# Performance work log

Measured on AMD Instinct MI355X. Metric: run time of the kernel, lower is better.

## Reference

```python
import jax, jax.numpy as jnp
import numpy as np

C = 512; H = 64; W = 64; STRIDE = 16; NA = 9; IMG = 1024
PRE_NMS = 6000; POST_NMS = 300; NMS_T = 0.7; MIN_SIZE = 16.0
BBOX_CLIP = float(np.log(1000.0 / 16.0))  # standard dw/dh clamp for exp() safety


def _make_anchors():
    # 3 scales x 3 aspect ratios on a stride-16 grid -> (H*W*9, 4) xyxy anchors
    scales = np.array([128.0, 256.0, 512.0])
    ratios = np.array([0.5, 1.0, 2.0])
    hs = (scales[:, None] * np.sqrt(ratios)[None, :]).ravel()
    ws = (scales[:, None] / np.sqrt(ratios)[None, :]).ravel()
    yy, xx = np.meshgrid((np.arange(H) + 0.5) * STRIDE, (np.arange(W) + 0.5) * STRIDE, indexing='ij')
    ctr = np.stack([xx.ravel(), yy.ravel()], -1)            # (HW, 2) centers
    wh = np.stack([ws, hs], -1)                              # (9, 2)
    anc = np.concatenate([ctr[:, None, :] - 0.5 * wh[None], ctr[:, None, :] + 0.5 * wh[None]], -1)
    return anc.reshape(-1, 4).astype(np.float32)             # (HW*9, 4)


def setup_inputs() -> dict:
    key = jax.random.key(0)
    k = jax.random.split(key, 4)
    return {
        'feature_map': jax.random.normal(k[0], (1, C, H, W), jnp.float32),
        'anchors': jnp.asarray(_make_anchors()),
        'image_shape': jnp.array([IMG, IMG], jnp.int32),
        'conv1_w': 0.01 * jax.random.normal(k[1], (C, C, 3, 3), jnp.float32),
        'conv1_b': jnp.zeros((C,), jnp.float32),
        'cls_w': 0.01 * jax.random.normal(k[2], (NA, C, 1, 1), jnp.float32),
        'cls_b': jnp.zeros((NA,), jnp.float32),
        'box_w': 0.01 * jax.random.normal(k[3], (NA * 4, C, 1, 1), jnp.float32),
        'box_b': jnp.zeros((NA * 4,), jnp.float32),
    }


def _conv(x, w, b):
    dn = ('NCHW', 'OIHW', 'NCHW')
    return jax.lax.conv_general_dilated(x, w, (1, 1), 'SAME', dimension_numbers=dn) + b[None, :, None, None]


def _decode_boxes(deltas, anchors):
    aw = anchors[:, 2] - anchors[:, 0]
    ah = anchors[:, 3] - anchors[:, 1]
    ax = anchors[:, 0] + 0.5 * aw
    ay = anchors[:, 1] + 0.5 * ah
    dx, dy, dw, dh = deltas[:, 0], deltas[:, 1], deltas[:, 2], deltas[:, 3]
    dw = jnp.minimum(dw, BBOX_CLIP)
    dh = jnp.minimum(dh, BBOX_CLIP)
    px = dx * aw + ax
    py = dy * ah + ay
    pw = jnp.exp(dw) * aw
    ph = jnp.exp(dh) * ah
    return jnp.stack([px - 0.5 * pw, py - 0.5 * ph, px + 0.5 * pw, py + 0.5 * ph], -1)


def _pairwise_iou(a, b):
    area_a = (a[:, 2] - a[:, 0]) * (a[:, 3] - a[:, 1])
    area_b = (b[:, 2] - b[:, 0]) * (b[:, 3] - b[:, 1])
    lt = jnp.maximum(a[:, None, :2], b[None, :, :2])
    rb = jnp.minimum(a[:, None, 2:], b[None, :, 2:])
    wh = jnp.clip(rb - lt, 0.0)
    inter = wh[..., 0] * wh[..., 1]
    union = area_a[:, None] + area_b[None, :] - inter
    return jnp.where(union > 0, inter / union, 0.0)


def reference(feature_map, anchors, image_shape, conv1_w, conv1_b, cls_w, cls_b, box_w, box_b):
    # conv head
    y = jax.nn.relu(_conv(feature_map, conv1_w, conv1_b))
    scores = _conv(y, cls_w, cls_b).reshape(-1)            # (H*W*9,)  torch .view(-1) order
    deltas = _conv(y, box_w, box_b).reshape(-1, 4)         # (H*W*9, 4) torch .reshape(-1,4) order
    preds = _decode_boxes(deltas, anchors)

    # filter_proposals: sigmoid -> topk 6000 -> clamp -> min-size -> NMS(0.7) -> top 300
    s = jax.nn.sigmoid(scores)
    topv, topi = jax.lax.top_k(s, PRE_NMS)                  # sorted descending
    b = preds[topi]
    h_img = image_shape[0].astype(jnp.float32)
    w_img = image_shape[1].astype(jnp.float32)
    b = jnp.stack([jnp.clip(b[:, 0], 0.0, w_img), jnp.clip(b[:, 1], 0.0, h_img),
                   jnp.clip(b[:, 2], 0.0, w_img), jnp.clip(b[:, 3], 0.0, h_img)], -1)
    valid = ((b[:, 2] - b[:, 0]) >= MIN_SIZE) & ((b[:, 3] - b[:, 1]) >= MIN_SIZE)

    iou = _pairwise_iou(b, b)                               # (6000, 6000)
    idx = jnp.arange(PRE_NMS)

    def body(i, keep):  # greedy NMS in score order (boxes already sorted desc)
        sup = (iou[i] > NMS_T) & keep[i] & (idx > i)
        return keep & (~sup)

    keep = jax.lax.fori_loop(0, PRE_NMS, body, valid)
    fs = jnp.where(keep, topv, -1.0)                        # suppressed/invalid -> sentinel
    sc, i2 = jax.lax.top_k(fs, POST_NMS)
    return b[i2], sc
```

## Files before the change

### kernel.cpp

```cpp
#include <hip/hip_runtime.h>
#include <hip/hip_bf16.h>

typedef unsigned int u32;
typedef unsigned long long u64;
typedef float v2f __attribute__((ext_vector_type(2)));
typedef float v4f __attribute__((ext_vector_type(4)));

#define OFF_Y      0ull
#define OFF_WT     8388608ull
#define OFF_ZPART  8388608ull
#define OFF_SCORES 11337728ull
#define OFF_DRAW   11485184ull
#define OFF_HIST   12075008ull
#define OFF_TOPV   12665344ull
#define OFF_BOXES  12714496ull
#define OFF_VW     12812800ull
#define OFF_MASK   12813824ull

#define NS     36864
#define PRE    6000
#define POST   300
#define SORTN  8192
#define MROW   96
#define NBW    8

__global__ __launch_bounds__(256) void k_wtrans(const float* __restrict__ gw,
                                                float* __restrict__ wT) {
    __shared__ float tile[64][65];
    const int t = threadIdx.x;
    const int tr = t & 63;
    const int tc = t >> 6;
    const int bco = (blockIdx.x & 7) << 6;
    const int brr = (blockIdx.x >> 3) << 6;

#pragma unroll
    for (int i = 0; i < 16; ++i) {
        int row = tc + (i << 2);
        tile[row][tr] = gw[(size_t)(bco + row) * 4608 + brr + tr];
    }
    __syncthreads();
#pragma unroll
    for (int i = 0; i < 16; ++i) {
        int rl = tc + (i << 2);
        int rg = brr + rl;
        int ci = rg / 9;
        int k = rg - ci * 9;
        wT[(size_t)ci * 4608 + k * 512 + bco + tr] = tile[tr][rl];
    }
}

__device__ __forceinline__ float dpp_shr1(float v) {
    return __int_as_float(__builtin_amdgcn_update_dpp(
        0, __float_as_int(v), 0x138, 0xF, 0xF, true));
}
__device__ __forceinline__ float dpp_shl1(float v) {
    return __int_as_float(__builtin_amdgcn_update_dpp(
        0, __float_as_int(v), 0x130, 0xF, 0xF, true));
}
__global__ __launch_bounds__(256, 4) void k_conv1(const float* __restrict__ x,
                                                  const float* __restrict__ wT,
                                                  const float* __restrict__ gb,
                                                  float* __restrict__ y) {
    const int t = threadIdx.x;
    const int tx = t & 63;
    const int wv = __builtin_amdgcn_readfirstlane(t >> 6);
    const int cob = (blockIdx.x & 15) << 5;
    const int h0 = blockIdx.x >> 4;
    const int co_base = cob + (wv << 3);

    const bool rv0 = (h0 > 0);
    const bool rv2 = (h0 < 63);
    const float* xp0 = x + (rv0 ? (h0 - 1) : h0) * 64 + tx;
    const float* xp1 = x + h0 * 64 + tx;
    const float* xp2 = x + (rv2 ? (h0 + 1) : h0) * 64 + tx;

    v2f acc2[4];
#pragma unroll
    for (int j = 0; j < 4; ++j) acc2[j] = (v2f){0.f, 0.f};

#pragma unroll 2
    for (int ci = 0; ci < 512; ++ci) {
        float c0 = xp0[(size_t)ci * 4096];
        float c1 = xp1[(size_t)ci * 4096];
        float c2 = xp2[(size_t)ci * 4096];
        c0 = rv0 ? c0 : 0.f;
        c2 = rv2 ? c2 : 0.f;
        float xr[9];
        xr[0] = dpp_shr1(c0); xr[1] = c0; xr[2] = dpp_shl1(c0);
        xr[3] = dpp_shr1(c1); xr[4] = c1; xr[5] = dpp_shl1(c1);
        xr[6] = dpp_shr1(c2); xr[7] = c2; xr[8] = dpp_shl1(c2);

        const v2f* wk2 = (const v2f*)(wT + (size_t)ci * 4608 + co_base);
#pragma unroll
        for (int k = 0; k < 9; ++k) {
            v2f w0 = wk2[k * 256 + 0];
            v2f w1 = wk2[k * 256 + 1];
            v2f w2 = wk2[k * 256 + 2];
            v2f w3 = wk2[k * 256 + 3];
            float xv = xr[k];
            v2f xpv = {xv, xv};
            acc2[0] = __builtin_elementwise_fma(w0, xpv, acc2[0]);
            acc2[1] = __builtin_elementwise_fma(w1, xpv, acc2[1]);
            acc2[2] = __builtin_elementwise_fma(w2, xpv, acc2[2]);
            acc2[3] = __builtin_elementwise_fma(w3, xpv, acc2[3]);
        }
    }

#pragma unroll
    for (int j = 0; j < 4; ++j) {
        int co0 = co_base + 2 * j;
        float v0 = acc2[j].x + gb[co0];
        float v1 = acc2[j].y + gb[co0 + 1];
        v0 = v0 > 0.f ? v0 : 0.f;
        v1 = v1 > 0.f ? v1 : 0.f;
        y[co0 * 4096 + (h0 << 6) + tx] = v0;
        y[(co0 + 1) * 4096 + (h0 << 6) + tx] = v1;
    }
}

__global__ __launch_bounds__(256) void k_heads_part(const float* __restrict__ y,
                                                    const float* __restrict__ cw,
                                                    const float* __restrict__ bw,
                                                    float* __restrict__ zpart,
                                                    u32* __restrict__ hist) {
    __shared__ __align__(16) float ys[64][132];
    const int t = threadIdx.x;
    {
        int hb = blockIdx.x << 9;
        hist[hb + t] = 0u;
        hist[hb + 256 + t] = 0u;
    }
    const int px = t & 63;
    const int gu = __builtin_amdgcn_readfirstlane(t >> 6);
    const int px0 = (blockIdx.x & 63) << 6;
    const int q = blockIdx.x >> 6;
    const int cib = q << 7;
    const int nch = (gu == 0) ? 12 : 11;

    const float* wrow[12];
#pragma unroll
    for (int j = 0; j < 12; ++j) {
        int ch = gu + 4 * j;
        if (ch < 9) wrow[j] = cw + ch * 512;
        else if (ch < 45) wrow[j] = bw + (ch - 9) * 512;
        else wrow[j] = cw;
    }
    float acc[12];
#pragma unroll
    for (int j = 0; j < 12; ++j) acc[j] = 0.f;

    for (int idx = t; idx < 128 * 64; idx += 256) {
        int ci = idx >> 6;
        int pp = idx & 63;
        ys[pp][ci] = y[(cib + ci) * 4096 + px0 + pp];
    }
    __syncthreads();

#pragma unroll 1
    for (int cq = 0; cq < 32; ++cq) {
        float4 yv = *(const float4*)&ys[px][cq << 2];
        float4 wv[12];
#pragma unroll
        for (int j = 0; j < 12; ++j)
            if (j < nch) wv[j] = *(const float4*)(wrow[j] + cib + (cq << 2));
#pragma unroll
        for (int j = 0; j < 12; ++j)
            if (j < nch)
                acc[j] += wv[j].x * yv.x + wv[j].y * yv.y + wv[j].z * yv.z + wv[j].w * yv.w;
    }
    for (int j = 0; j < nch; ++j) {
        int ch = gu + 4 * j;
        zpart[((q * 45 + ch) << 12) + px0 + px] = acc[j];
    }
}

__global__ __launch_bounds__(256) void k_hreduce(const float* __restrict__ zpart,
                                                 const float* __restrict__ cb,
                                                 const float* __restrict__ bb,
                                                 float* __restrict__ scores,
                                                 float* __restrict__ draw,
                                                 u32* __restrict__ hist) {
    int i = blockIdx.x * 256 + threadIdx.x;
    if (i >= 45 * 4096) return;
    int ch = i >> 12;
    int sp = i & 4095;
    float z = zpart[((0 * 45 + ch) << 12) + sp] + zpart[((1 * 45 + ch) << 12) + sp] +
              zpart[((2 * 45 + ch) << 12) + sp] + zpart[((3 * 45 + ch) << 12) + sp];
    if (ch < 9) {
        z += cb[ch];
        float s = 1.f / (1.f + expf(-z));
        scores[(ch << 12) + sp] = s;
        u32 sb = __float_as_uint(s);
        atomicAdd(&hist[sb >> 13], 1u);
    } else {
        z += bb[ch - 9];
        draw[((ch - 9) << 12) + sp] = z;
    }
}

__global__ __launch_bounds__(1024) void k_select(const u32* __restrict__ hist,
                                                 const float* __restrict__ scores,
                                                 const float* __restrict__ draw,
                                                 const float* __restrict__ anchors,
                                                 const int* __restrict__ ishape,
                                                 float* __restrict__ boxes,
                                                 float* __restrict__ topv,
                                                 u64* __restrict__ vw) {
    __shared__ u32 csum[1024];
    __shared__ u32 suf[1024];
    __shared__ u64 sk[SORTN];
    __shared__ int sel_s, cnt_s;
    const int t = threadIdx.x;

    u32 s = 0;
    {
        const uint4* hp4 = (const uint4*)(hist + t * 128);
#pragma unroll 4
        for (int i = 0; i < 32; ++i) {
            uint4 h4 = hp4[i];
            s += h4.x + h4.y + h4.z + h4.w;
        }
    }
    csum[t] = s;
    suf[t] = s;
    if (t == 0) cnt_s = 0;
    __syncthreads();
    for (int off = 1; off < 1024; off <<= 1) {
        u32 v = suf[t] + ((t + off < 1024) ? suf[t + off] : 0u);
        __syncthreads();
        suf[t] = v;
        __syncthreads();
    }
    u32 above = suf[t] - csum[t];
    if (above < (u32)PRE && suf[t] >= (u32)PRE) {
        const u32* hp = hist + t * 128;
        u32 run = above;
        int bstar = t * 128;
        u32 found = 0;
        for (int b2 = 127; b2 >= 0; --b2) {
            u32 c = hp[b2];
            if (!found && run + c >= (u32)PRE) { bstar = t * 128 + b2; found = 1; }
            if (!found) run += c;
        }
        sel_s = bstar;
    }
    for (int i = t; i < SORTN; i += 1024) sk[i] = 0;
    __syncthreads();

    const int sel = sel_s;
#pragma unroll 1
    for (int u = 0; u < 9; ++u) {
        int g = t + (u << 10);
        float4 s4 = *(const float4*)(scores + (g << 2));
#pragma unroll
        for (int e = 0; e < 4; ++e) {
            u32 sb = __float_as_uint(((const float*)&s4)[e]);
            if ((int)(sb >> 13) >= sel) {
                int p = atomicAdd(&cnt_s, 1);
                if (p < SORTN) sk[p] = ((u64)sb << 32) | (u32)(~((g << 2) + e));
            }
        }
    }
    __syncthreads();

    const int base = t << 3;
    u64 a[8];
    {
#pragma unroll
        for (int u = 0; u < 8; ++u) a[u] = sk[base + u];
#pragma unroll
        for (int k = 2; k <= 8; k <<= 1) {
#pragma unroll
            for (int j = k >> 1; j > 0; j >>= 1) {
#pragma unroll
                for (int u = 0; u < 8; ++u) {
                    if ((u & j) == 0) {
                        int l = u | j;
                        bool up = (((base + u) & k) == 0);
                        u64 x0 = a[u], x1 = a[l];
                        if (up ? (x0 < x1) : (x0 > x1)) { a[u] = x1; a[l] = x0; }
                    }
                }
            }
        }
#pragma unroll
        for (int u = 0; u < 8; ++u) sk[base + u] = a[u];
        __syncthreads();
    }
    for (int k = 16; k <= SORTN; k <<= 1) {
        for (int j = k >> 1; j >= 8; j >>= 1) {
#pragma unroll
            for (int s2 = 0; s2 < 4; ++s2) {
                int pidx = t + (s2 << 10);
                int i = ((pidx & ~(j - 1)) << 1) | (pidx & (j - 1));
                int l = i | j;
                u64 x0 = sk[i], x1 = sk[l];
                bool up = ((i & k) == 0);
                if (up ? (x0 < x1) : (x0 > x1)) { sk[i] = x1; sk[l] = x0; }
            }
            __syncthreads();
        }
#pragma unroll
        for (int u = 0; u < 8; ++u) a[u] = sk[base + u];
        {
            bool up = ((base & k) == 0);
#pragma unroll
            for (int j = 4; j > 0; j >>= 1) {
#pragma unroll
                for (int u = 0; u < 8; ++u) {
                    if ((u & j) == 0) {
                        int l = u | j;
                        u64 x0 = a[u], x1 = a[l];
                        if (up ? (x0 < x1) : (x0 > x1)) { a[u] = x1; a[l] = x0; }
                    }
                }
            }
        }
#pragma unroll
        for (int u = 0; u < 8; ++u) sk[base + u] = a[u];
        __syncthreads();
    }

    const float wimg = (float)ishape[1], himg = (float)ishape[0];
#pragma unroll 1
    for (int s2 = 0; s2 < 6; ++s2) {
        int r = (s2 << 10) + t;
        bool valid = false;
        if (r < PRE) {
            u64 key = sk[r];
            u32 sb = (u32)(key >> 32);
            int i = (int)(~(u32)key);
            topv[r] = __uint_as_float(sb);
            int c = i >> 10;
            int t4 = i & 1023;
            float4 d4 = *(const float4*)(draw + c * 4096 + (t4 << 2));
            float4 a4 = *(const float4*)(anchors + i * 4);
            float aw = a4.z - a4.x, ah = a4.w - a4.y;
            float ax = a4.x + 0.5f * aw, ay = a4.y + 0.5f * ah;
            const float CLIPV = (float)4.135166556742356;
            float dw = fminf(d4.z, CLIPV);
            float dh = fminf(d4.w, CLIPV);
            float px = d4.x * aw + ax, py = d4.y * ah + ay;
            float pw = expf(dw) * aw, ph = expf(dh) * ah;
            float x1 = fminf(fmaxf(px - 0.5f * pw, 0.f), wimg);
            float y1 = fminf(fmaxf(py - 0.5f * ph, 0.f), himg);
            float x2 = fminf(fmaxf(px + 0.5f * pw, 0.f), wimg);
            float y2 = fminf(fmaxf(py + 0.5f * ph, 0.f), himg);
            valid = (x2 - x1 >= 16.f) && (y2 - y1 >= 16.f);
            *(float4*)(boxes + r * 4) = make_float4(x1, y1, x2, y2);
        }
        u64 bm = __ballot(valid);
        if ((t & 63) == 0) vw[(s2 << 4) + (t >> 6)] = bm;
    }
}

__global__ __launch_bounds__(256) void k_mask(const float* __restrict__ boxes,
                                              u64* __restrict__ mask) {
    __shared__ float4 cbx[16 * 65];
    const int t = threadIdx.x;
    const int r0 = blockIdx.x << 4;
    const int row = r0 + (t >> 4);
    const int wloc = t & 15;
    float4 rb = *(const float4*)(boxes + row * 4);
    float area_a = (rb.z - rb.x) * (rb.w - rb.y);
    for (int chunk = 0; chunk < 6; ++chunk) {
        int j0c = chunk << 10;
        for (int idx = t; idx < 1024; idx += 256) {
            int j = j0c + idx;
            float4 v = make_float4(0.f, 0.f, 0.f, 0.f);
            if (j < PRE) v = *(const float4*)(boxes + j * 4);
            cbx[(idx >> 6) * 65 + (idx & 63)] = v;
        }
        __syncthreads();
        u64 bits = 0;
        const float4* cbr = cbx + wloc * 65;
        for (int b = 0; b < 64; ++b) {
            int j = j0c + (wloc << 6) + b;
            float4 ob = cbr[b];
            float area_b = (ob.z - ob.x) * (ob.w - ob.y);
            float ltx = fmaxf(rb.x, ob.x), lty = fmaxf(rb.y, ob.y);
            float rbx = fminf(rb.z, ob.z), rby = fminf(rb.w, ob.w);
            float wx = fmaxf(rbx - ltx, 0.f), wy = fmaxf(rby - lty, 0.f);
            float inter = wx * wy;
            float uni = area_a + area_b - inter;
            float iou = (uni > 0.f) ? (inter / uni) : 0.f;
            if (iou > 0.7f && j > row && j < PRE) bits |= (1ull << b);
        }
        mask[(size_t)row * MROW + (chunk << 4) + wloc] = bits;
        __syncthreads();
    }
}

__device__ __forceinline__ u64 readlane64(u64 v, int lane) {
    u32 lo = (u32)__builtin_amdgcn_readlane((int)(u32)v, lane);
    u32 hi = (u32)__builtin_amdgcn_readlane((int)(u32)(v >> 32), lane);
    return ((u64)hi << 32) | lo;
}
__global__ __launch_bounds__(320) void k_nms_out(const u64* __restrict__ mask,
                                                 const u64* __restrict__ vw,
                                                 const float* __restrict__ boxes,
                                                 const float* __restrict__ topv,
                                                 float* __restrict__ out) {
    __shared__ u64 kws[MROW];
    __shared__ int keepl[POST];
    __shared__ int kc_s;
    const int tid = threadIdx.x;
    if (tid < MROW) kws[tid] = 0ull;
    __syncthreads();

    if (tid < 64) {
        const int lane = tid;
        u64 vw0 = (lane < 94) ? vw[lane] : 0ull;
        u64 vw1 = (lane < 30) ? vw[64 + lane] : 0ull;
        u64 rem0 = 0ull, rem1 = 0ull;
        int kc = 0;
        bool done = false;
        for (int w = 0; w < 94 && !done; ++w) {
            u64 vww  = (w < 64) ? readlane64(vw0, w)  : readlane64(vw1, w - 64);
            u64 remw = (w < 64) ? readlane64(rem0, w) : readlane64(rem1, w - 64);
            u64 aw = vww & ~remw;
            u64 kwbits = 0;
            while (aw && !done) {
                int bq[NBW];
                u64 tmp = aw;
#pragma unroll
                for (int q = 0; q < NBW; ++q) {
                    bq[q] = tmp ? __builtin_ctzll(tmp) : 64;
                    tmp &= tmp - 1;
                }
                u64 rq0[NBW], rq1[NBW];
#pragma unroll
                for (int q = 0; q < NBW; ++q) {
                    rq0[q] = 0ull; rq1[q] = 0ull;
                    if (bq[q] < 64) {
                        const u64* mrow = mask + (size_t)((w << 6) + bq[q]) * MROW;
                        rq0[q] = mrow[lane];
                        if (lane < 30) rq1[q] = mrow[64 + lane];
                    }
                }
#pragma unroll
                for (int q = 0; q < NBW; ++q) {
                    int b = bq[q];
                    if (b >= 64) break;
                    if (!((aw >> b) & 1ull)) continue;
                    if (lane == 0) keepl[kc] = (w << 6) + b;
                    kc++;
                    kwbits |= (1ull << b);
                    if (kc >= POST) { done = true; break; }
                    rem0 |= rq0[q];
                    rem1 |= rq1[q];
                    u64 roww = (w < 64) ? readlane64(rq0[q], w) : readlane64(rq1[q], w - 64);
                    aw &= ~roww;
                    aw &= ~(1ull << b);
                }
            }
            if (lane == 0) kws[w] = kwbits;
        }
        if (lane == 0) kc_s = kc;
    }
    __syncthreads();

    int j = tid;
    if (j >= POST) return;
    int kc2 = kc_s;
    int r;
    float sc;
    if (j < kc2) {
        r = keepl[j];
        sc = topv[r];
    } else {
        int target = j - kc2;
        r = PRE - 1;
        int cum = 0;
        for (int w = 0; w < 94; ++w) {
            u64 kb = kws[w];
            int nvalid = (w < 93) ? 64 : 48;
            u64 vmask2 = (nvalid == 64) ? ~0ull : ((1ull << nvalid) - 1ull);
            u64 nk = (~kb) & vmask2;
            int c = __popcll(nk);
            if (cum + c > target) {
                int need = target - cum;
                u64 m = nk;
                for (int q = 0; q < need; ++q) m &= (m - 1);
                r = (w << 6) + __builtin_ctzll(m);
                break;
            }
            cum += c;
        }
        sc = -1.0f;
    }
    out[j * 4 + 0] = boxes[r * 4 + 0];
    out[j * 4 + 1] = boxes[r * 4 + 1];
    out[j * 4 + 2] = boxes[r * 4 + 2];
    out[j * 4 + 3] = boxes[r * 4 + 3];
    out[1200 + j] = sc;
}

extern "C" void kernel_launch(void* const* d_in, const int* in_sizes, int n_in,
                              void* d_out, int out_size, void* d_ws, size_t ws_size,
                              hipStream_t stream) {
    const float* x = (const float*)d_in[0];
    const float* anchors = (const float*)d_in[1];
    const int* ishape = (const int*)d_in[2];
    const float* c1w = (const float*)d_in[3];
    const float* c1b = (const float*)d_in[4];
    const float* clw = (const float*)d_in[5];
    const float* clb = (const float*)d_in[6];
    const float* bxw = (const float*)d_in[7];
    const float* bxb = (const float*)d_in[8];

    char* ws = (char*)d_ws;
    float* y      = (float*)(ws + OFF_Y);
    float* wT     = (float*)(ws + OFF_WT);
    float* zpart  = (float*)(ws + OFF_ZPART);
    float* scores = (float*)(ws + OFF_SCORES);
    float* draw   = (float*)(ws + OFF_DRAW);
    u32*   hist   = (u32*)(ws + OFF_HIST);
    float* topv   = (float*)(ws + OFF_TOPV);
    float* boxes  = (float*)(ws + OFF_BOXES);
    u64*   vw     = (u64*)(ws + OFF_VW);
    u64*   mask   = (u64*)(ws + OFF_MASK);

    k_wtrans<<<576, 256, 0, stream>>>(c1w, wT);
    k_conv1<<<1024, 256, 0, stream>>>(x, wT, c1b, y);
    k_heads_part<<<256, 256, 0, stream>>>(y, clw, bxw, zpart, hist);
    k_hreduce<<<(45 * 4096 + 255) / 256, 256, 0, stream>>>(zpart, clb, bxb, scores, draw, hist);
    k_select<<<1, 1024, 0, stream>>>(hist, scores, draw, anchors, ishape, boxes, topv, vw);
    k_mask<<<PRE / 16, 256, 0, stream>>>(boxes, mask);
    k_nms_out<<<1, 320, 0, stream>>>(mask, vw, boxes, topv, (float*)d_out);
}
```

Baseline: 645.0 us.

## Replace shared-memory bitonic sort with histogram counting sort plus in-bin ranking

The single-block select kernel no longer runs a full bitonic sort over 8192 keys. It turns the score histogram in place into exclusive descending prefix offsets, scatters each candidate to its bin slot with atomics on those global counters, then ranks each key only against keys in the same bin and writes it to a second shared buffer. This removes the many barrier-separated bitonic passes. In exchange it adds contended global atomics, doubles shared-memory use, mutates the histogram buffer, and has a per-element cost that grows quadratically if many scores land in one bin.

```diff
diff --git a/kernel.cpp b/kernel.cpp
--- a/kernel.cpp
+++ b/kernel.cpp
@@ -198,7 +198,7 @@
     }
 }
 
-__global__ __launch_bounds__(1024) void k_select(const u32* __restrict__ hist,
+__global__ __launch_bounds__(1024) void k_select(const u32* __restrict__ hist_c,
                                                  const float* __restrict__ scores,
                                                  const float* __restrict__ draw,
                                                  const float* __restrict__ anchors,
@@ -206,10 +206,12 @@
                                                  float* __restrict__ boxes,
                                                  float* __restrict__ topv,
                                                  u64* __restrict__ vw) {
+    u32* hist = (u32*)hist_c;
     __shared__ u32 csum[1024];
     __shared__ u32 suf[1024];
     __shared__ u64 sk[SORTN];
-    __shared__ int sel_s, cnt_s;
+    __shared__ u64 sk2[SORTN];
+    __shared__ int sel_s, tot_s;
     const int t = threadIdx.x;
 
     u32 s = 0;
@@ -223,7 +225,6 @@
     }
     csum[t] = s;
     suf[t] = s;
-    if (t == 0) cnt_s = 0;
     __syncthreads();
     for (int off = 1; off < 1024; off <<= 1) {
         u32 v = suf[t] + ((t + off < 1024) ? suf[t + off] : 0u);
@@ -244,7 +245,28 @@
         }
         sel_s = bstar;
     }
-    for (int i = t; i < SORTN; i += 1024) sk[i] = 0;
+    {
+        const int base = t << 7;
+        u32 runv = above;
+#pragma unroll 1
+        for (int c = 7; c >= 0; --c) {
+            uint4 a[4];
+#pragma unroll
+            for (int q = 0; q < 4; ++q)
+                a[q] = *(const uint4*)(hist + base + c * 16 + q * 4);
+            u32 nv[16];
+#pragma unroll
+            for (int i = 15; i >= 0; --i) {
+                u32 cntv = ((u32*)a)[i];
+                nv[i] = runv;
+                runv += cntv;
+            }
+#pragma unroll
+            for (int q = 0; q < 4; ++q)
+                *(uint4*)(hist + base + c * 16 + q * 4) =
+                    make_uint4(nv[q * 4], nv[q * 4 + 1], nv[q * 4 + 2], nv[q * 4 + 3]);
+        }
+    }
     __syncthreads();
 
     const int sel = sel_s;
@@ -255,71 +277,39 @@
 #pragma unroll
         for (int e = 0; e < 4; ++e) {
             u32 sb = __float_as_uint(((const float*)&s4)[e]);
-            if ((int)(sb >> 13) >= sel) {
-                int p = atomicAdd(&cnt_s, 1);
-                if (p < SORTN) sk[p] = ((u64)sb << 32) | (u32)(~((g << 2) + e));
+            int bin = (int)(sb >> 13);
+            if (bin >= sel) {
+                u32 slot = atomicAdd(&hist[bin], 1u);
+                if (slot < (u32)SORTN)
+                    sk[slot] = ((u64)sb << 32) | (u32)(~((g << 2) + e));
             }
         }
     }
     __syncthreads();
-
-    const int base = t << 3;
-    u64 a[8];
-    {
-#pragma unroll
-        for (int u = 0; u < 8; ++u) a[u] = sk[base + u];
-#pragma unroll
-        for (int k = 2; k <= 8; k <<= 1) {
-#pragma unroll
-            for (int j = k >> 1; j > 0; j >>= 1) {
-#pragma unroll
-                for (int u = 0; u < 8; ++u) {
-                    if ((u & j) == 0) {
-                        int l = u | j;
-                        bool up = (((base + u) & k) == 0);
-                        u64 x0 = a[u], x1 = a[l];
-                        if (up ? (x0 < x1) : (x0 > x1)) { a[u] = x1; a[l] = x0; }
-                    }
-                }
-            }
-        }
-#pragma unroll
-        for (int u = 0; u < 8; ++u) sk[base + u] = a[u];
-        __syncthreads();
-    }
-    for (int k = 16; k <= SORTN; k <<= 1) {
-        for (int j = k >> 1; j >= 8; j >>= 1) {
-#pragma unroll
-            for (int s2 = 0; s2 < 4; ++s2) {
-                int pidx = t + (s2 << 10);
-                int i = ((pidx & ~(j - 1)) << 1) | (pidx & (j - 1));
-                int l = i | j;
-                u64 x0 = sk[i], x1 = sk[l];
-                bool up = ((i & k) == 0);
-                if (up ? (x0 < x1) : (x0 > x1)) { sk[i] = x1; sk[l] = x0; }
-            }
-            __syncthreads();
-        }
-#pragma unroll
-        for (int u = 0; u < 8; ++u) a[u] = sk[base + u];
-        {
-            bool up = ((base & k) == 0);
-#pragma unroll
-            for (int j = 4; j > 0; j >>= 1) {
-#pragma unroll
-                for (int u = 0; u < 8; ++u) {
-                    if ((u & j) == 0) {
-                        int l = u | j;
-                        u64 x0 = a[u], x1 = a[l];
-                        if (up ? (x0 < x1) : (x0 > x1)) { a[u] = x1; a[l] = x0; }
-                    }
-                }
-            }
-        }
-#pragma unroll
-        for (int u = 0; u < 8; ++u) sk[base + u] = a[u];
-        __syncthreads();
-    }
+    if (t == 0) tot_s = (int)hist[sel];
+    __syncthreads();
+
+    const int total = (tot_s < SORTN) ? tot_s : SORTN;
+#pragma unroll 1
+    for (int r = t; r < total; r += 1024) {
+        u64 e = sk[r];
+        u32 b = (u32)(e >> 45);
+        int rank = 0;
+        int pos0 = r;
+        for (int q = r - 1; q >= 0; --q) {
+            u64 f = sk[q];
+            if ((u32)(f >> 45) != b) break;
+            pos0 = q;
+            if (f > e) ++rank;
+        }
+        for (int q = r + 1; q < total; ++q) {
+            u64 f = sk[q];
+            if ((u32)(f >> 45) != b) break;
+            if (f > e) ++rank;
+        }
+        sk2[pos0 + rank] = e;
+    }
+    __syncthreads();
 
     const float wimg = (float)ishape[1], himg = (float)ishape[0];
 #pragma unroll 1
@@ -327,7 +317,7 @@
         int r = (s2 << 10) + t;
         bool valid = false;
         if (r < PRE) {
-            u64 key = sk[r];
+            u64 key = sk2[r];
             u32 sb = (u32)(key >> 32);
             int i = (int)(~(u32)key);
             topv[r] = __uint_as_float(sb);
```

Result: slower. 765.2 us (+18.6%).
